# Kernel tuning notes

Hardware: AMD Instinct MI355X
Metric: run time of the kernel (lower is better)

## Reference

```python
import jax, jax.numpy as jnp
import numpy as np

B, N, C, H = 2, 2048, 1024, 16
D = C // H          # head dim = 64
HID = 4 * C         # MLP hidden = 4096
LN_EPS = 1e-5
ROPE_BASE = 10000.0


def layernorm(x, g, b):
    mu = jnp.mean(x, axis=-1, keepdims=True)
    var = jnp.var(x, axis=-1, keepdims=True)
    return (x - mu) * jax.lax.rsqrt(var + LN_EPS) * g + b


def rotate_half(x):
    # interleaved pairs: (x0, x1) -> (-x1, x0), lucidrains rotary_embedding_torch style
    x = x.reshape(*x.shape[:-1], -1, 2)
    x1, x2 = x[..., 0], x[..., 1]
    return jnp.stack([-x2, x1], axis=-1).reshape(*x.shape[:-2], -1)


def rope_cos_sin(n, d, dtype):
    inv_freq = 1.0 / (ROPE_BASE ** (jnp.arange(0, d, 2, dtype=jnp.float32) / d))
    ang = jnp.arange(n, dtype=jnp.float32)[:, None] * inv_freq          # [N, D/2]
    ang = jnp.repeat(ang, 2, axis=-1)                                    # [N, D] interleaved
    return jnp.cos(ang).astype(dtype), jnp.sin(ang).astype(dtype)


def setup_inputs() -> dict:
    key = jax.random.key(0)
    ks = jax.random.split(key, 16)
    s = 0.02
    return {
        "x": jax.random.normal(ks[0], (B, N, C), jnp.float32),
        "ln1_g": jnp.ones((C,), jnp.float32),
        "ln1_b": jnp.zeros((C,), jnp.float32),
        "qkv_w": jax.random.normal(ks[1], (C, 3 * C), jnp.float32) * s,   # stored [in, out]
        "qkv_b": jnp.zeros((3 * C,), jnp.float32),
        "proj_w": jax.random.normal(ks[2], (C, C), jnp.float32) * s,
        "proj_b": jnp.zeros((C,), jnp.float32),
        "ln2_g": jnp.ones((C,), jnp.float32),
        "ln2_b": jnp.zeros((C,), jnp.float32),
        "fc1_w": jax.random.normal(ks[3], (C, HID), jnp.float32) * s,
        "fc1_b": jnp.zeros((HID,), jnp.float32),
        "ffn_ln_g": jnp.ones((HID,), jnp.float32),
        "ffn_ln_b": jnp.zeros((HID,), jnp.float32),
        "fc2_w": jax.random.normal(ks[4], (HID, C), jnp.float32) * s,
        "fc2_b": jnp.zeros((C,), jnp.float32),
    }


def reference(x, ln1_g, ln1_b, qkv_w, qkv_b, proj_w, proj_b,
              ln2_g, ln2_b, fc1_w, fc1_b, ffn_ln_g, ffn_ln_b, fc2_w, fc2_b):
    b, n, c = x.shape
    h, d = H, c // H
    scale = d ** -0.5

    # --- attention branch (pre-norm) ---
    hx = layernorm(x, ln1_g, ln1_b)
    qkv = hx @ qkv_w + qkv_b                                   # [B,N,3C]
    qkv = qkv.reshape(b, n, 3, h, d).transpose(2, 0, 3, 1, 4)  # [3,B,H,N,D]
    q, k, v = qkv[0], qkv[1], qkv[2]

    cos, sin = rope_cos_sin(n, d, x.dtype)                     # [N,D]
    q = q * cos + rotate_half(q) * sin
    k = k * cos + rotate_half(k) * sin

    attn = jax.nn.softmax(jnp.einsum('bhqd,bhkd->bhqk', q, k) * scale, axis=-1)
    o = jnp.einsum('bhqk,bhkd->bhqd', attn, v)                 # [B,H,N,D]
    o = o.transpose(0, 2, 1, 3).reshape(b, n, c)               # B N (H D)
    x = x + o @ proj_w + proj_b

    # --- MLP branch (pre-norm; GELU then LayerNorm on hidden, per FeedForwardBlock) ---
    m = layernorm(x, ln2_g, ln2_b)
    m = jax.nn.gelu(m @ fc1_w + fc1_b, approximate=False)
    m = layernorm(m, ffn_ln_g, ffn_ln_b)
    m = m @ fc2_w + fc2_b
    return x + m
```

## Files before the change

kernel.cpp:

```cpp
#include <hip/hip_runtime.h>
#include <hip/hip_bf16.h>
#include <cmath>

typedef __bf16 bf16_t;
typedef __bf16 bf16x8 __attribute__((ext_vector_type(8)));
typedef float f32x4 __attribute__((ext_vector_type(4)));
typedef float f32x16 __attribute__((ext_vector_type(16)));
typedef unsigned short u16;
typedef unsigned int u32;

#if defined(__has_builtin)
#if __has_builtin(__builtin_amdgcn_exp2f)
#define ATTN_EXP(x) __builtin_amdgcn_exp2f(x)
#define ATTN_LOG2E 1.4426950408889634f
#endif
#endif
#ifndef ATTN_EXP
#define ATTN_EXP(x) __expf(x)
#define ATTN_LOG2E 1.0f
#endif

__device__ __forceinline__ void load16(const bf16_t* g, bf16_t* l) {
  __builtin_amdgcn_global_load_lds((const __attribute__((address_space(1))) u32*)g,
                                   (__attribute__((address_space(3))) u32*)l, 16, 0, 0);
}

__device__ __forceinline__ u32 pk2(float a, float b) {
  bf16_t x = (bf16_t)a, y = (bf16_t)b;
  u16 ux = __builtin_bit_cast(u16, x), uy = __builtin_bit_cast(u16, y);
  return (u32)ux | ((u32)uy << 16);
}

union V4U { u32 w[4]; bf16x8 v; };

__device__ __forceinline__ void tr64(const float* __restrict__ src, bf16_t* __restrict__ dst,
                                     int Kd, int Nd, int ntile, int ktile, int tid) {
  __shared__ float tile[64][68];
  int n0 = ntile * 64, k0 = ktile * 64;
  int r = tid >> 2, c4 = (tid & 3) * 4;
  const float* sp = src + (size_t)(k0 + r) * Nd + n0;
#pragma unroll
  for (int c = 0; c < 4; ++c)
    *(float4*)&tile[r][c * 16 + c4] = *(const float4*)(sp + c * 16 + c4);
  __syncthreads();
  int n = tid >> 2;
  bf16_t* dp = dst + (size_t)(n0 + n) * Kd + k0;
#pragma unroll
  for (int c = 0; c < 4; ++c) {
    int kk = c * 16 + c4;
    uint2 pk;
    pk.x = pk2(tile[kk + 0][n], tile[kk + 1][n]);
    pk.y = pk2(tile[kk + 2][n], tile[kk + 3][n]);
    *(uint2*)(dp + kk) = pk;
  }
}

__global__ __launch_bounds__(256) void prep_kernel(
    const float* __restrict__ qkv_w, const float* __restrict__ proj_w,
    const float* __restrict__ fc1_w, const float* __restrict__ fc2_w,
    bf16_t* __restrict__ qkvT, bf16_t* __restrict__ projT,
    bf16_t* __restrict__ fc1T, bf16_t* __restrict__ fc2T,
    float* __restrict__ ropeC, float* __restrict__ ropeS) {
  int b = blockIdx.x, tid = threadIdx.x;
  if (b < 768) {
    tr64(qkv_w, qkvT, 1024, 3072, b % 48, b / 48, tid);
  } else if (b < 1024) {
    int r = b - 768; tr64(proj_w, projT, 1024, 1024, r % 16, r / 16, tid);
  } else if (b < 2048) {
    int r = b - 1024; tr64(fc1_w, fc1T, 1024, 4096, r % 64, r / 64, tid);
  } else if (b < 3072) {
    int r = b - 2048; tr64(fc2_w, fc2T, 4096, 1024, r % 16, r / 16, tid);
  } else {
    int idx = (b - 3072) * 256 + tid;
    int pos = idx >> 5, t = idx & 31;
    float e = (float)(2 * t) / 64.0f;
    float inv = powf(10000.0f, -e);
    float a = (float)pos * inv;
    ropeC[idx] = cosf(a);
    ropeS[idx] = sinf(a);
  }
}

template <typename TI, int W>
__global__ __launch_bounds__(256) void ln_kernel(const TI* __restrict__ in,
                                                 const float* __restrict__ g,
                                                 const float* __restrict__ b,
                                                 bf16_t* __restrict__ out) {
  constexpr int PT = W / 256;
  int row = blockIdx.x;
  const TI* p = in + (size_t)row * W;
  float vals[PT];
  float s = 0.f, q = 0.f;
  for (int i = 0; i < PT; ++i) {
    float v = (float)p[threadIdx.x + i * 256];
    vals[i] = v; s += v; q += v * v;
  }
  for (int off = 32; off; off >>= 1) { s += __shfl_xor(s, off); q += __shfl_xor(q, off); }
  __shared__ float red[8];
  int wave = threadIdx.x >> 6, lane = threadIdx.x & 63;
  if (lane == 0) { red[wave] = s; red[4 + wave] = q; }
  __syncthreads();
  s = red[0] + red[1] + red[2] + red[3];
  q = red[4] + red[5] + red[6] + red[7];
  float mu = s * (1.0f / W);
  float var = q * (1.0f / W) - mu * mu;
  float rstd = rsqrtf(var + 1e-5f);
  bf16_t* op = out + (size_t)row * W;
  for (int i = 0; i < PT; ++i) {
    int cix = threadIdx.x + i * 256;
    op[cix] = (bf16_t)((vals[i] - mu) * rstd * g[cix] + b[cix]);
  }
}

enum { EPI_QKV = 0, EPI_RESID = 1, EPI_GELU = 2 };

template <int EPI, int TM>
__global__ __launch_bounds__(256, 2) void gemm_bt(
    const bf16_t* __restrict__ A, const bf16_t* __restrict__ Bt, int M, int Nn, int K,
    int gy,
    const float* __restrict__ bias, const float* __restrict__ resid,
    float* __restrict__ outf, bf16_t* __restrict__ outb,
    bf16_t* __restrict__ qb, bf16_t* __restrict__ kb, bf16_t* __restrict__ vtb,
    const float* __restrict__ ropeC, const float* __restrict__ ropeS) {
  constexpr int MT = TM / 32;
  __shared__ bf16_t lsA[2][TM * 32];
  __shared__ bf16_t lsB[2][128 * 32];
  const int tid = threadIdx.x;
  const int lane = tid & 63;
  const int wave = tid >> 6;
  const int l16 = lane & 15, quad = lane >> 4;
  const int wm = (wave >> 1) * (TM / 2), wn = (wave & 1) * 64;
  const int bb = blockIdx.x;
  const int m0 = (bb % gy) * TM, n0 = (bb / gy) * 128;

  f32x4 acc[MT][4];
  for (int i = 0; i < MT; ++i)
    for (int j = 0; j < 4; ++j) acc[i][j] = {0.f, 0.f, 0.f, 0.f};

  auto stage = [&](int kk, int buf) {
    bf16_t* la = &lsA[buf][0];
    bf16_t* lb = &lsB[buf][0];
#pragma unroll
    for (int i = 0; i < TM / 64; ++i) {
      int s = tid + i * 256;
      int row = s >> 2, ch = (s & 3) ^ (row & 3);
      load16(A + (size_t)(m0 + row) * K + kk + ch * 8, la + s * 8);
    }
#pragma unroll
    for (int i = 0; i < 2; ++i) {
      int s = tid + i * 256;
      int row = s >> 2, ch = (s & 3) ^ (row & 3);
      load16(Bt + (size_t)(n0 + row) * K + kk + ch * 8, lb + s * 8);
    }
  };

  const int nk = K >> 5;
  stage(0, 0);
  for (int ki = 0; ki < nk; ++ki) {
    __syncthreads();
    if (ki + 1 < nk) stage((ki + 1) << 5, (ki + 1) & 1);
    const bf16_t* la = &lsA[ki & 1][0];
    const bf16_t* lb = &lsB[ki & 1][0];
    bf16x8 af[MT], bfr[4];
#pragma unroll
    for (int t = 0; t < MT; ++t) {
      int row = wm + t * 16 + l16;
      af[t] = *(const bf16x8*)(la + row * 32 + (quad ^ (row & 3)) * 8);
    }
#pragma unroll
    for (int t = 0; t < 4; ++t) {
      int row = wn + t * 16 + l16;
      bfr[t] = *(const bf16x8*)(lb + row * 32 + (quad ^ (row & 3)) * 8);
    }
#pragma unroll
    for (int mt = 0; mt < MT; ++mt)
#pragma unroll
      for (int nt = 0; nt < 4; ++nt)
        acc[mt][nt] = __builtin_amdgcn_mfma_f32_16x16x32_bf16(af[mt], bfr[nt], acc[mt][nt], 0, 0, 0);
  }

  for (int mt = 0; mt < MT; ++mt) {
    for (int nt = 0; nt < 4; ++nt) {
      int gn = n0 + wn + nt * 16 + l16;
      int gm0 = m0 + wm + mt * 16 + quad * 4;
      if constexpr (EPI == EPI_QKV) {
        int which = gn >> 10;
        int hd = gn & 1023, head = hd >> 6, d = hd & 63;
        if (which == 2) {
          u32 lo, hi;
          {
            float v0 = acc[mt][nt][0] + bias[gn];
            float v1 = acc[mt][nt][1] + bias[gn];
            float v2 = acc[mt][nt][2] + bias[gn];
            float v3 = acc[mt][nt][3] + bias[gn];
            lo = pk2(v0, v1);
            hi = pk2(v2, v3);
          }
          int b = gm0 >> 11, pos = gm0 & 2047;
          int bh = b * 16 + head;
          uint2 pk; pk.x = lo; pk.y = hi;
          *(uint2*)(vtb + ((size_t)bh * 64 + d) * 2048 + pos) = pk;
        } else {
          bf16_t* dst = (which == 0) ? qb : kb;
          int t = d >> 1;
          for (int r = 0; r < 4; ++r) {
            float v = acc[mt][nt][r] + bias[gn];
            float pn = __shfl_xor(v, 1);
            int gm = gm0 + r;
            int b = gm >> 11, pos = gm & 2047;
            float cc = ropeC[pos * 32 + t], ss = ropeS[pos * 32 + t];
            float o = (d & 1) ? (v * cc + pn * ss) : (v * cc - pn * ss);
            dst[(((size_t)(b * 16 + head)) * 2048 + pos) * 64 + d] = (bf16_t)o;
          }
        }
      } else if constexpr (EPI == EPI_GELU) {
        for (int r = 0; r < 4; ++r) {
          int gm = gm0 + r;
          float v = acc[mt][nt][r] + bias[gn];
          float g = 0.5f * v * (1.0f + erff(v * 0.70710678118654752f));
          outb[(size_t)gm * Nn + gn] = (bf16_t)g;
        }
      } else {
        for (int r = 0; r < 4; ++r) {
          int gm = gm0 + r;
          size_t idx = (size_t)gm * Nn + gn;
          outf[idx] = acc[mt][nt][r] + bias[gn] + resid[idx];
        }
      }
    }
  }
}

__global__ __launch_bounds__(256, 2) void attn_kernel(
    const bf16_t* __restrict__ q, const bf16_t* __restrict__ k,
    const bf16_t* __restrict__ vt, bf16_t* __restrict__ o) {
  __shared__ bf16_t lsK[2][128 * 64];
  __shared__ bf16_t lsV[2][64 * 128];

  const int tid = threadIdx.x, lane = tid & 63, wave = tid >> 6;
  const int c31 = lane & 31, hi = lane >> 5, h7 = c31 & 7;
  const int bh = blockIdx.y, qt = blockIdx.x;
  const int b = bh >> 4, h = bh & 15;
  const bf16_t* qp = q + (size_t)bh * 2048 * 64;
  const bf16_t* kp = k + (size_t)bh * 2048 * 64;
  const bf16_t* vp = vt + (size_t)bh * 64 * 2048;
  const int qrow0 = qt * 128 + wave * 32;
  const int qrow = qrow0 + c31;

  const float QS = 0.125f * ATTN_LOG2E;
  bf16x8 qb[4];
#pragma unroll
  for (int ks = 0; ks < 4; ++ks) {
    bf16x8 t = *(const bf16x8*)(qp + (size_t)qrow * 64 + ks * 16 + hi * 8);
#pragma unroll
    for (int j = 0; j < 8; ++j) t[j] = (bf16_t)((float)t[j] * QS);
    qb[ks] = t;
  }

  f32x16 oacc[2];
  oacc[0] = 0.f; oacc[1] = 0.f;
  float mstate = -3.0e38f, lstate = 0.f;

  auto stage = [&](int kt, int buf) {
    const bf16_t* kg = kp + (size_t)kt * 128 * 64;
    bf16_t* lk = &lsK[buf][0];
    bf16_t* lv = &lsV[buf][0];
#pragma unroll
    for (int i = 0; i < 4; ++i) {
      int s = tid + i * 256;
      int kr = s >> 3, kc = (s & 7) ^ (kr & 7);
      load16(kg + (size_t)kr * 64 + kc * 8, lk + s * 8);
      int vr = s >> 4, vc = (s & 15) ^ (vr & 7);
      load16(vp + (size_t)vr * 2048 + kt * 128 + vc * 8, lv + s * 8);
    }
  };

  stage(0, 0);
  for (int kt = 0; kt < 16; ++kt) {
    __syncthreads();
    if (kt < 15) stage(kt + 1, (kt + 1) & 1);
    const bf16_t* lk = &lsK[kt & 1][0];
    const bf16_t* lv = &lsV[kt & 1][0];

    f32x16 sacc[4];
    sacc[0] = 0.f; sacc[1] = 0.f; sacc[2] = 0.f; sacc[3] = 0.f;
#pragma unroll
    for (int ks = 0; ks < 4; ++ks) {
      int cs = ((ks * 2 + hi) ^ h7) * 8;
#pragma unroll
      for (int nt = 0; nt < 4; ++nt) {
        bf16x8 kf = *(const bf16x8*)(lk + (nt * 32 + c31) * 64 + cs);
        sacc[nt] = __builtin_amdgcn_mfma_f32_32x32x16_bf16(kf, qb[ks], sacc[nt], 0, 0, 0);
      }
    }

    float mx = sacc[0][0];
#pragma unroll
    for (int nt = 0; nt < 4; ++nt)
#pragma unroll
      for (int r = 0; r < 16; ++r) mx = fmaxf(mx, sacc[nt][r]);
    mx = fmaxf(mx, __shfl_xor(mx, 32));
    float mnew = fmaxf(mstate, mx);
    float alpha = ATTN_EXP(mstate - mnew);
    mstate = mnew;
    float rs = 0.f;
    u32 u[4][4][2];
#pragma unroll
    for (int nt = 0; nt < 4; ++nt)
#pragma unroll
      for (int t = 0; t < 4; ++t) {
        float p0 = ATTN_EXP(sacc[nt][4 * t + 0] - mnew);
        float p1 = ATTN_EXP(sacc[nt][4 * t + 1] - mnew);
        float p2 = ATTN_EXP(sacc[nt][4 * t + 2] - mnew);
        float p3 = ATTN_EXP(sacc[nt][4 * t + 3] - mnew);
        rs += (p0 + p1) + (p2 + p3);
        u[nt][t][0] = pk2(p0, p1);
        u[nt][t][1] = pk2(p2, p3);
      }
    rs += __shfl_xor(rs, 32);
    lstate = lstate * alpha + rs;
#pragma unroll
    for (int dt = 0; dt < 2; ++dt)
#pragma unroll
      for (int r = 0; r < 16; ++r) oacc[dt][r] *= alpha;

#pragma unroll
    for (int ks = 0; ks < 8; ++ks) {
      int n = ks >> 1, t0 = (ks & 1) * 2;
      u32 a0 = u[n][t0][0], a1 = u[n][t0][1];
      u32 b0 = u[n][t0 + 1][0], b1 = u[n][t0 + 1][1];
      u32 ax0 = (u32)__shfl_xor((int)a0, 32), ax1 = (u32)__shfl_xor((int)a1, 32);
      u32 bx0 = (u32)__shfl_xor((int)b0, 32), bx1 = (u32)__shfl_xor((int)b1, 32);
      V4U f;
      f.w[0] = hi ? bx0 : a0;
      f.w[1] = hi ? bx1 : a1;
      f.w[2] = hi ? b0 : ax0;
      f.w[3] = hi ? b1 : ax1;
      bf16x8 pf = f.v;
      int cs = ((ks * 2 + hi) ^ h7) * 8;
#pragma unroll
      for (int dt = 0; dt < 2; ++dt) {
        bf16x8 vf = *(const bf16x8*)(lv + (dt * 32 + c31) * 128 + cs);
        oacc[dt] = __builtin_amdgcn_mfma_f32_32x32x16_bf16(vf, pf, oacc[dt], 0, 0, 0);
      }
    }
  }

  float inv = 1.0f / lstate;
  bf16_t* orow = o + ((size_t)(b * 2048 + qrow)) * 1024 + h * 64;
#pragma unroll
  for (int dt = 0; dt < 2; ++dt)
#pragma unroll
    for (int t = 0; t < 4; ++t) {
      int d0 = dt * 32 + 8 * t + 4 * hi;
      uint2 pk;
      pk.x = pk2(oacc[dt][4 * t + 0] * inv, oacc[dt][4 * t + 1] * inv);
      pk.y = pk2(oacc[dt][4 * t + 2] * inv, oacc[dt][4 * t + 3] * inv);
      *(uint2*)(orow + d0) = pk;
    }
}

extern "C" void kernel_launch(void* const* d_in, const int* in_sizes, int n_in,
                              void* d_out, int out_size, void* d_ws, size_t ws_size,
                              hipStream_t stream) {
  const float* x = (const float*)d_in[0];
  const float* ln1_g = (const float*)d_in[1];
  const float* ln1_b = (const float*)d_in[2];
  const float* qkv_w = (const float*)d_in[3];
  const float* qkv_b = (const float*)d_in[4];
  const float* proj_w = (const float*)d_in[5];
  const float* proj_b = (const float*)d_in[6];
  const float* ln2_g = (const float*)d_in[7];
  const float* ln2_b = (const float*)d_in[8];
  const float* fc1_w = (const float*)d_in[9];
  const float* fc1_b = (const float*)d_in[10];
  const float* ffg = (const float*)d_in[11];
  const float* ffb = (const float*)d_in[12];
  const float* fc2_w = (const float*)d_in[13];
  const float* fc2_b = (const float*)d_in[14];
  float* out = (float*)d_out;

  char* ws = (char*)d_ws;
  size_t off = 0;
  auto alloc = [&](size_t n) { char* p = ws + off; off += (n + 255) & ~(size_t)255; return p; };

  bf16_t* qkvT  = (bf16_t*)alloc(3072ull * 1024 * 2);
  bf16_t* projT = (bf16_t*)alloc(1024ull * 1024 * 2);
  bf16_t* fc1T  = (bf16_t*)alloc(4096ull * 1024 * 2);
  bf16_t* fc2T  = (bf16_t*)alloc(1024ull * 4096 * 2);
  float*  ropeC = (float*)alloc(2048ull * 32 * 4);
  float*  ropeS = (float*)alloc(2048ull * 32 * 4);
  bf16_t* hx    = (bf16_t*)alloc(4096ull * 1024 * 2);
  bf16_t* qbuf  = (bf16_t*)alloc(32ull * 2048 * 64 * 2);
  bf16_t* kbuf  = (bf16_t*)alloc(32ull * 2048 * 64 * 2);
  bf16_t* vtbuf = (bf16_t*)alloc(32ull * 64 * 2048 * 2);
  bf16_t* obuf  = (bf16_t*)alloc(4096ull * 1024 * 2);
  float*  x2    = (float*)alloc(4096ull * 1024 * 4);
  bf16_t* h1    = (bf16_t*)alloc(4096ull * 4096 * 2);
  bf16_t* hln   = (bf16_t*)qbuf;

  prep_kernel<<<3328, 256, 0, stream>>>(qkv_w, proj_w, fc1_w, fc2_w,
                                        qkvT, projT, fc1T, fc2T, ropeC, ropeS);

  ln_kernel<float, 1024><<<4096, 256, 0, stream>>>(x, ln1_g, ln1_b, hx);
  gemm_bt<EPI_QKV, 128><<<768, 256, 0, stream>>>(hx, qkvT, 4096, 3072, 1024, 32, qkv_b,
      nullptr, nullptr, nullptr, qbuf, kbuf, vtbuf, ropeC, ropeS);
  attn_kernel<<<dim3(16, 32), 256, 0, stream>>>(qbuf, kbuf, vtbuf, obuf);
  gemm_bt<EPI_RESID, 64><<<512, 256, 0, stream>>>(obuf, projT, 4096, 1024, 1024, 64, proj_b,
      x, x2, nullptr, nullptr, nullptr, nullptr, nullptr, nullptr);
  ln_kernel<float, 1024><<<4096, 256, 0, stream>>>(x2, ln2_g, ln2_b, hx);
  gemm_bt<EPI_GELU, 128><<<1024, 256, 0, stream>>>(hx, fc1T, 4096, 4096, 1024, 32, fc1_b,
      nullptr, nullptr, h1, nullptr, nullptr, nullptr, nullptr, nullptr);
  ln_kernel<bf16_t, 4096><<<4096, 256, 0, stream>>>(h1, ffg, ffb, hln);
  gemm_bt<EPI_RESID, 64><<<512, 256, 0, stream>>>(hln, fc2T, 4096, 1024, 4096, 64, fc2_b,
      x2, out, nullptr, nullptr, nullptr, nullptr, nullptr, nullptr);
}
```

Measured before the change: 391.5 us.

## Split-K atomic GEMMs for projections with residual pre-init in LayerNorm

The proj and fc2 GEMMs switch to split-K (2 and 4 splits) with 128-row tiles and accumulate into fp32 outputs with atomic adds. Those outputs are pre-initialised by the preceding LayerNorm kernels, which now also write residual plus bias. The LayerNorm kernels are vectorised to float4 and bf16x8 loads with packed stores. This aims to improve occupancy and CU utilisation on the N=1024 GEMMs and to drop the separate residual read. In exchange it adds atomic traffic, an extra fp32 write in LN, and non-deterministic summation order.

```diff
diff --git a/kernel.cpp b/kernel.cpp
--- a/kernel.cpp
+++ b/kernel.cpp
@@ -85,15 +85,33 @@
 __global__ __launch_bounds__(256) void ln_kernel(const TI* __restrict__ in,
                                                  const float* __restrict__ g,
                                                  const float* __restrict__ b,
-                                                 bf16_t* __restrict__ out) {
-  constexpr int PT = W / 256;
+                                                 bf16_t* __restrict__ out,
+                                                 const float* __restrict__ aux_b,
+                                                 float* __restrict__ aux_out) {
+  constexpr int CH = (sizeof(TI) == 2) ? 8 : 4;
+  constexpr int NS = W / (256 * CH);
   int row = blockIdx.x;
   const TI* p = in + (size_t)row * W;
-  float vals[PT];
+  float vals[NS * CH];
   float s = 0.f, q = 0.f;
-  for (int i = 0; i < PT; ++i) {
-    float v = (float)p[threadIdx.x + i * 256];
-    vals[i] = v; s += v; q += v * v;
+#pragma unroll
+  for (int sw = 0; sw < NS; ++sw) {
+    int base = sw * (256 * CH) + threadIdx.x * CH;
+    if constexpr (sizeof(TI) == 2) {
+      bf16x8 v = *(const bf16x8*)(p + base);
+#pragma unroll
+      for (int e = 0; e < 8; ++e) {
+        float f = (float)v[e];
+        vals[sw * CH + e] = f; s += f; q += f * f;
+      }
+    } else {
+      float4 v = *(const float4*)(p + base);
+      float f0 = v.x, f1 = v.y, f2 = v.z, f3 = v.w;
+      vals[sw * CH + 0] = f0; vals[sw * CH + 1] = f1;
+      vals[sw * CH + 2] = f2; vals[sw * CH + 3] = f3;
+      s += (f0 + f1) + (f2 + f3);
+      q += (f0 * f0 + f1 * f1) + (f2 * f2 + f3 * f3);
+    }
   }
   for (int off = 32; off; off >>= 1) { s += __shfl_xor(s, off); q += __shfl_xor(q, off); }
   __shared__ float red[8];
@@ -106,18 +124,36 @@
   float var = q * (1.0f / W) - mu * mu;
   float rstd = rsqrtf(var + 1e-5f);
   bf16_t* op = out + (size_t)row * W;
-  for (int i = 0; i < PT; ++i) {
-    int cix = threadIdx.x + i * 256;
-    op[cix] = (bf16_t)((vals[i] - mu) * rstd * g[cix] + b[cix]);
-  }
-}
-
-enum { EPI_QKV = 0, EPI_RESID = 1, EPI_GELU = 2 };
+#pragma unroll
+  for (int sw = 0; sw < NS; ++sw) {
+    int base = sw * (256 * CH) + threadIdx.x * CH;
+    float o[CH];
+#pragma unroll
+    for (int e = 0; e < CH; ++e)
+      o[e] = (vals[sw * CH + e] - mu) * rstd * g[base + e] + b[base + e];
+    if constexpr (CH == 8) {
+      V4U u;
+      u.w[0] = pk2(o[0], o[1]); u.w[1] = pk2(o[2], o[3]);
+      u.w[2] = pk2(o[4], o[5]); u.w[3] = pk2(o[6], o[7]);
+      *(bf16x8*)(op + base) = u.v;
+    } else {
+      uint2 pk; pk.x = pk2(o[0], o[1]); pk.y = pk2(o[2], o[3]);
+      *(uint2*)(op + base) = pk;
+    }
+    if (aux_out) {
+      float* ap = aux_out + (size_t)row * W + base;
+#pragma unroll
+      for (int e = 0; e < CH; ++e) ap[e] = vals[sw * CH + e] + aux_b[base + e];
+    }
+  }
+}
+
+enum { EPI_QKV = 0, EPI_RESID = 1, EPI_GELU = 2, EPI_ATOMIC = 3 };
 
 template <int EPI, int TM>
 __global__ __launch_bounds__(256, 2) void gemm_bt(
     const bf16_t* __restrict__ A, const bf16_t* __restrict__ Bt, int M, int Nn, int K,
-    int gy,
+    int gy, int ksteps,
     const float* __restrict__ bias, const float* __restrict__ resid,
     float* __restrict__ outf, bf16_t* __restrict__ outb,
     bf16_t* __restrict__ qb, bf16_t* __restrict__ kb, bf16_t* __restrict__ vtb,
@@ -132,6 +168,7 @@
   const int wm = (wave >> 1) * (TM / 2), wn = (wave & 1) * 64;
   const int bb = blockIdx.x;
   const int m0 = (bb % gy) * TM, n0 = (bb / gy) * 128;
+  const int kbase = blockIdx.y * (ksteps << 5);
 
   f32x4 acc[MT][4];
   for (int i = 0; i < MT; ++i)
@@ -154,11 +191,10 @@
     }
   };
 
-  const int nk = K >> 5;
-  stage(0, 0);
-  for (int ki = 0; ki < nk; ++ki) {
+  stage(kbase, 0);
+  for (int ki = 0; ki < ksteps; ++ki) {
     __syncthreads();
-    if (ki + 1 < nk) stage((ki + 1) << 5, (ki + 1) & 1);
+    if (ki + 1 < ksteps) stage(kbase + ((ki + 1) << 5), (ki + 1) & 1);
     const bf16_t* la = &lsA[ki & 1][0];
     const bf16_t* lb = &lsB[ki & 1][0];
     bf16x8 af[MT], bfr[4];
@@ -220,6 +256,11 @@
           float g = 0.5f * v * (1.0f + erff(v * 0.70710678118654752f));
           outb[(size_t)gm * Nn + gn] = (bf16_t)g;
         }
+      } else if constexpr (EPI == EPI_ATOMIC) {
+        for (int r = 0; r < 4; ++r) {
+          int gm = gm0 + r;
+          unsafeAtomicAdd(outf + (size_t)gm * Nn + gn, acc[mt][nt][r]);
+        }
       } else {
         for (int r = 0; r < 4; ++r) {
           int gm = gm0 + r;
@@ -402,16 +443,16 @@
   prep_kernel<<<3328, 256, 0, stream>>>(qkv_w, proj_w, fc1_w, fc2_w,
                                         qkvT, projT, fc1T, fc2T, ropeC, ropeS);
 
-  ln_kernel<float, 1024><<<4096, 256, 0, stream>>>(x, ln1_g, ln1_b, hx);
-  gemm_bt<EPI_QKV, 128><<<768, 256, 0, stream>>>(hx, qkvT, 4096, 3072, 1024, 32, qkv_b,
+  ln_kernel<float, 1024><<<4096, 256, 0, stream>>>(x, ln1_g, ln1_b, hx, proj_b, x2);
+  gemm_bt<EPI_QKV, 128><<<768, 256, 0, stream>>>(hx, qkvT, 4096, 3072, 1024, 32, 32, qkv_b,
       nullptr, nullptr, nullptr, qbuf, kbuf, vtbuf, ropeC, ropeS);
   attn_kernel<<<dim3(16, 32), 256, 0, stream>>>(qbuf, kbuf, vtbuf, obuf);
-  gemm_bt<EPI_RESID, 64><<<512, 256, 0, stream>>>(obuf, projT, 4096, 1024, 1024, 64, proj_b,
-      x, x2, nullptr, nullptr, nullptr, nullptr, nullptr, nullptr);
-  ln_kernel<float, 1024><<<4096, 256, 0, stream>>>(x2, ln2_g, ln2_b, hx);
-  gemm_bt<EPI_GELU, 128><<<1024, 256, 0, stream>>>(hx, fc1T, 4096, 4096, 1024, 32, fc1_b,
+  gemm_bt<EPI_ATOMIC, 128><<<dim3(256, 2), 256, 0, stream>>>(obuf, projT, 4096, 1024, 1024,
+      32, 16, nullptr, nullptr, x2, nullptr, nullptr, nullptr, nullptr, nullptr, nullptr);
+  ln_kernel<float, 1024><<<4096, 256, 0, stream>>>(x2, ln2_g, ln2_b, hx, fc2_b, out);
+  gemm_bt<EPI_GELU, 128><<<1024, 256, 0, stream>>>(hx, fc1T, 4096, 4096, 1024, 32, 32, fc1_b,
       nullptr, nullptr, h1, nullptr, nullptr, nullptr, nullptr, nullptr);
-  ln_kernel<bf16_t, 4096><<<4096, 256, 0, stream>>>(h1, ffg, ffb, hln);
-  gemm_bt<EPI_RESID, 64><<<512, 256, 0, stream>>>(hln, fc2T, 4096, 1024, 4096, 64, fc2_b,
-      x2, out, nullptr, nullptr, nullptr, nullptr, nullptr, nullptr);
-}
+  ln_kernel<bf16_t, 4096><<<4096, 256, 0, stream>>>(h1, ffg, ffb, hln, nullptr, nullptr);
+  gemm_bt<EPI_ATOMIC, 128><<<dim3(256, 4), 256, 0, stream>>>(hln, fc2T, 4096, 1024, 4096,
+      32, 32, nullptr, nullptr, out, nullptr, nullptr, nullptr, nullptr, nullptr, nullptr);
+}
```

After: 417.4 us. 1.07x slower.
